# Optimization experiments

Measured on AMD Instinct MI355X. Metric: run time of the kernel, lower is better.

Reference implementation:

```python
import jax, jax.numpy as jnp
import numpy as np

B, N, DIM = 8, 2048, 1024
EPSILON = 0.03
SCALE = 1.0 / np.sqrt(DIM).astype(np.float32)


def setup_inputs() -> dict:
    key = jax.random.key(0)
    ks = jax.random.split(key, 5)
    Q = jax.random.normal(ks[0], (B, N, DIM), dtype=jnp.float32)
    K = jax.random.normal(ks[1], (B, N, DIM), dtype=jnp.float32)
    V = jax.random.normal(ks[2], (B, N, DIM), dtype=jnp.float32)
    # H_net: Linear(dim, dim//2) -> SiLU -> Linear(dim//2, 1); init like torch default scale-ish
    W1 = jax.random.normal(ks[3], (DIM, DIM // 2), dtype=jnp.float32) * (1.0 / np.sqrt(DIM))
    b1 = jnp.zeros((DIM // 2,), dtype=jnp.float32)
    W2 = jax.random.normal(ks[4], (DIM // 2, 1), dtype=jnp.float32) * (1.0 / np.sqrt(DIM // 2))
    b2 = jnp.zeros((1,), dtype=jnp.float32)
    return {"Q": Q, "K": K, "V": V, "W1": W1, "b1": b1, "W2": W2, "b2": b2}


def _mlp(x, W1, b1, W2, b2):
    h = jax.nn.silu(x @ W1 + b1)  # [B,N,dim//2]
    return h @ W2 + b2            # [B,N,1]


def reference(Q, K, V, W1, b1, W2, b2):
    def energy(q, v):
        # scores [B,N,N]
        A = jax.nn.softmax(jnp.einsum('bnd,bmd->bnm', q, K) * SCALE, axis=-1)
        attn_out = jnp.einsum('bnm,bmd->bnd', A, v)
        H = jnp.sum(_mlp(attn_out, W1, b1, W2, b2))
        return H, attn_out

    # grads of scalar energy H w.r.t. Q and V (dH_dV is computed per the
    # original code but discarded by the final split; only dH_dQ survives)
    (dH_dQ, dH_dV), attn_out = jax.grad(energy, argnums=(0, 1), has_aux=True)(Q, V)
    # S_new = cat([Q,V]) + eps*cat([dH_dV, -dH_dQ]); split -> V_new = V - eps*dH_dQ
    V_new = V - EPSILON * dH_dQ
    return V_new + attn_out
```

## Files before the change

### kernel.cpp

```cpp
#include <hip/hip_runtime.h>

typedef __bf16 bf16;
typedef __attribute__((ext_vector_type(8))) __bf16 bf16x8;
typedef __attribute__((ext_vector_type(4))) float f32x4;

#define MEMFENCE asm volatile("" ::: "memory")

__device__ __forceinline__ void gload16(const bf16* g, bf16* l) {
    __builtin_amdgcn_global_load_lds(
        (const __attribute__((address_space(1))) void*)g,
        (__attribute__((address_space(3))) void*)l,
        16, 0, 0);
}

template<int EPI>
__global__ __launch_bounds__(512, 1)
void gemm8p(const bf16* __restrict__ A, const bf16* __restrict__ Bm,
            void* __restrict__ Cp, int Kdim, int lda, int ldb, int ldc,
            long sA, long sB, long sC, float alpha,
            const float* __restrict__ aux1, const bf16* __restrict__ aux3)
{
    __shared__ __align__(16) char smem[163840];

    const int gx = gridDim.x, gy = gridDim.y;
    int lin = blockIdx.x + gx * (blockIdx.y + gy * blockIdx.z);
    const int q = (gx * gy * gridDim.z) >> 3;
    lin = (lin & 7) * q + (lin >> 3);
    const int bx = lin % gx;
    const int rem0 = lin / gx;
    const int by = rem0 % gy;
    const int bz = rem0 / gy;

    const int t0 = threadIdx.x;
    const int w = t0 >> 6, lane = t0 & 63;
    const int wm = w >> 2, wn = w & 3;
    const int m0 = by * 256, n0 = bx * 256;
    const long zb = bz;

    const bf16* Ab = A  + zb * sA + (size_t)m0 * lda;
    const bf16* Bb = Bm + zb * sB + (size_t)n0 * ldb;

    const int sr16 = lane >> 2;
    const int sce  = ((((lane & 3) << 4) ^ (((lane >> 5) & 1) << 5))) >> 1;
    const int r0s = (w >> 1) * 16 + sr16;
    const int c0s = (w & 1) * 32 + sce;
    const bf16* gA0 = Ab + (size_t)r0s * lda + c0s;
    const bf16* gA1 = Ab + (size_t)(128 + r0s) * lda + c0s;
    const bf16* gB0 = Bb + (size_t)r0s * ldb + c0s;
    const bf16* gB1 = Bb + (size_t)(128 + r0s) * ldb + c0s;
    const size_t a64 = (size_t)64 * lda, b64 = (size_t)64 * ldb;
    const int ldsW0 = w * 1024, ldsW1 = (8 + w) * 1024;

    const int lr = lane & 15, lkq = lane >> 4;
    const int phx = ((lane >> 3) & 1) << 5;
    const int frag_base = (lr * 64 + lkq * 16) ^ phx;
    const char* aR = smem + wm * 16384 + frag_base;
    const char* bR = smem + 98304 + (wn >> 1) * 16384 + (wn & 1) * 8192 + frag_base;

    f32x4 acc[8][4] = {};
    const int NTt = Kdim >> 6;

    auto stgA = [&](int h, int u, int off) {
        char* L = smem + off + h * 16384;
        const bf16* g = h ? gA1 : gA0;
        gload16(g + (size_t)u * 64,        (bf16*)(L + ldsW0));
        gload16(g + a64 + (size_t)u * 64,  (bf16*)(L + ldsW1));
    };
    auto stgB = [&](int h, int u, int p) {
        char* L = smem + 98304 + p * 32768 + h * 16384;
        const bf16* g = h ? gB1 : gB0;
        gload16(g + (size_t)u * 64,        (bf16*)(L + ldsW0));
        gload16(g + b64 + (size_t)u * 64,  (bf16*)(L + ldsW1));
    };

    stgA(0, 0, 0);     stgA(1, 0, 0);     stgB(0, 0, 0); stgB(1, 0, 0);
    stgA(0, 1, 32768); stgA(1, 1, 32768); stgB(0, 1, 1); stgB(1, 1, 1);
    asm volatile("s_waitcnt vmcnt(8)" ::: "memory");
    __builtin_amdgcn_s_barrier();
    MEMFENCE;

    bf16x8 a[4][2], bl[2][2], bh[2][2];
    #pragma unroll
    for (int mf = 0; mf < 4; ++mf)
        #pragma unroll
        for (int ks = 0; ks < 2; ++ks)
            a[mf][ks] = *(const bf16x8*)(aR + (mf * 2 + ks) * 1024);
    #pragma unroll
    for (int nf = 0; nf < 2; ++nf)
        #pragma unroll
        for (int ks = 0; ks < 2; ++ks)
            bh[nf][ks] = *(const bf16x8*)(bR + ((2 + nf) * 2 + ks) * 1024);

#define QUADQ(MFB, NFB, AARR, BARR)                                                     \
    __builtin_amdgcn_s_setprio(1);                                                      \
    _Pragma("unroll")                                                                   \
    for (int ks = 0; ks < 2; ++ks)                                                      \
        _Pragma("unroll")                                                               \
        for (int mf = 0; mf < 4; ++mf)                                                  \
            _Pragma("unroll")                                                           \
            for (int nf = 0; nf < 2; ++nf)                                              \
                acc[(MFB) + mf][(NFB) + nf] = __builtin_amdgcn_mfma_f32_16x16x32_bf16(  \
                    AARR[mf][ks], BARR[nf][ks], acc[(MFB) + mf][(NFB) + nf], 0, 0, 0);  \
    __builtin_amdgcn_s_setprio(0);

    int aOff = 0, aOff1 = 32768, sOff = 65536;
    for (int u = 0; u < NTt; ++u) {
        const int p = u & 1;
        const char* aP  = aR + aOff;
        const char* aP1 = aR + aOff1;
        const char* bP  = bR + p * 32768;
        const char* bP1 = bR + (p ^ 1) * 32768;
        const bool st2 = (u + 2 < NTt), nx = (u + 1 < NTt);

        if (st2) stgA(0, u + 2, sOff);
        #pragma unroll
        for (int nf = 0; nf < 2; ++nf)
            #pragma unroll
            for (int ks = 0; ks < 2; ++ks)
                bl[nf][ks] = *(const bf16x8*)(bP + (nf * 2 + ks) * 1024);
        QUADQ(0, 2, a, bh)

        if (st2) stgA(1, u + 2, sOff);
        QUADQ(0, 0, a, bl)
        #pragma unroll
        for (int mf = 0; mf < 4; ++mf)
            #pragma unroll
            for (int ks = 0; ks < 2; ++ks)
                a[mf][ks] = *(const bf16x8*)(aP + ((4 + mf) * 2 + ks) * 1024);
        MEMFENCE;
        if (st2)     asm volatile("s_waitcnt vmcnt(4)" ::: "memory");
        else if (nx) asm volatile("s_waitcnt vmcnt(0)" ::: "memory");
        __builtin_amdgcn_s_barrier();
        MEMFENCE;

        if (st2) stgB(0, u + 2, p);
        QUADQ(4, 0, a, bl)

        if (st2) stgB(1, u + 2, p);
        QUADQ(4, 2, a, bh)
        if (nx) {
            #pragma unroll
            for (int mf = 0; mf < 4; ++mf)
                #pragma unroll
                for (int ks = 0; ks < 2; ++ks)
                    a[mf][ks] = *(const bf16x8*)(aP1 + (mf * 2 + ks) * 1024);
            #pragma unroll
            for (int nf = 0; nf < 2; ++nf)
                #pragma unroll
                for (int ks = 0; ks < 2; ++ks)
                    bh[nf][ks] = *(const bf16x8*)(bP1 + ((2 + nf) * 2 + ks) * 1024);
        }
        MEMFENCE;
        __builtin_amdgcn_s_barrier();
        MEMFENCE;

        const int tmp = aOff; aOff = aOff1; aOff1 = sOff; sOff = tmp;
    }
#undef QUADQ

    const int rb  = m0 + wm * 128 + lkq * 4;
    const int cb0 = n0 + wn * 64 + lr;
    #pragma unroll
    for (int mf = 0; mf < 8; ++mf) {
        #pragma unroll
        for (int r = 0; r < 4; ++r) {
            const int rw = rb + mf * 16 + r;
            float rd = 0.f;
            if (EPI == 1) rd = aux1[zb * 2048 + rw];
            #pragma unroll
            for (int nf = 0; nf < 4; ++nf) {
                const int c = cb0 + nf * 16;
                const size_t ix = (size_t)rw * ldc + c;
                const float v = acc[mf][nf][r];
                if (EPI == 0) {
                    ((bf16*)Cp + zb * sC)[ix] = (bf16)(alpha * v);
                } else if (EPI == 1) {
                    bf16* Cb = (bf16*)Cp + zb * sC;
                    const bf16* Am = aux3 + zb * sC;
                    Cb[ix] = (bf16)((float)Am[ix] * (v - rd));
                } else {
                    float* C = (float*)Cp + zb * sC;
                    const float* Vv = aux1 + zb * sC;
                    const bf16* AOv = aux3 + zb * sC;
                    C[ix] = Vv[ix] + (float)AOv[ix] - alpha * v;
                }
            }
        }
    }
}

template<int EPI, int NF>
__global__ __launch_bounds__(512, 1)
void gemm_nc(const bf16* __restrict__ A, const bf16* __restrict__ Bm,
             void* __restrict__ Cp, int Kdim, int lda, int ldb, int ldc,
             long sA, long sB, long sC, float alpha,
             const float* __restrict__ aux1, const float* __restrict__ aux2,
             const bf16* __restrict__ aux3)
{
    constexpr int SB = NF * 4096;
    __shared__ __align__(16) char smem[65536 + 4 * SB];

    const int gx = gridDim.x, gy = gridDim.y;
    int lin = blockIdx.x + gx * (blockIdx.y + gy * blockIdx.z);
    const int q = (gx * gy * gridDim.z) >> 3;
    lin = (lin & 7) * q + (lin >> 3);
    const int bx = lin % gx;
    const int rem0 = lin / gx;
    const int by = rem0 % gy;
    const int bz = rem0 / gy;

    const int t0 = threadIdx.x;
    const int w = t0 >> 6, lane = t0 & 63;
    const int wm = w >> 2, wn = w & 3;
    const int m0 = by * 256, n0 = bx * (64 * NF);
    const long zb = bz;

    const bf16* Ab = A  + zb * sA + (size_t)m0 * lda;
    const bf16* Bb = Bm + zb * sB + (size_t)n0 * ldb;

    const int sr16 = lane >> 2;
    const int sce  = ((((lane & 3) << 4) ^ (((lane >> 5) & 1) << 5))) >> 1;
    const int stg0 = w * 2, stg1 = w * 2 + 1;
    const bf16* pA0 = Ab + (size_t)(stg0 * 16 + sr16) * lda + sce;
    const bf16* pA1 = Ab + (size_t)(stg1 * 16 + sr16) * lda + sce;
    const bf16* pB0 = Bb + (size_t)((NF == 4 ? stg0 : w) * 16 + sr16) * ldb + sce;
    const bf16* pB1 = Bb + (size_t)(stg1 * 16 + sr16) * ldb + sce;

    const int lr = lane & 15, lkq = lane >> 4;
    const int phx = ((lane >> 3) & 1) << 5;
    const int frag_base = lr * 64 + lkq * 16;

    f32x4 acc[8][NF] = {};
    const int NT = Kdim >> 5;

    auto issueSlot = [&](int p) {
        char* lA = smem + (p & 3) * 16384;
        char* lB = smem + 65536 + (p & 3) * SB;
        const int kt = p << 5;
        gload16(pA0 + kt, (bf16*)(lA + stg0 * 1024));
        gload16(pA1 + kt, (bf16*)(lA + stg1 * 1024));
        if (NF == 4) {
            gload16(pB0 + kt, (bf16*)(lB + stg0 * 1024));
            gload16(pB1 + kt, (bf16*)(lB + stg1 * 1024));
        } else {
            gload16(pB0 + kt, (bf16*)(lB + w * 1024));
        }
    };
    auto rdA = [&](const char* base, int sub) {
        return *(const bf16x8*)(base + (((sub << 10) + frag_base) ^ phx));
    };

    issueSlot(0); issueSlot(1); issueSlot(2);
    if (NF == 4) asm volatile("s_waitcnt vmcnt(4)" ::: "memory");
    else         asm volatile("s_waitcnt vmcnt(3)" ::: "memory");
    __builtin_amdgcn_s_barrier();
    MEMFENCE;

    bf16x8 alo[4], ahi[4], b0[NF], b1[NF];
    {
        const char* cA = smem;
        const char* cB = smem + 65536;
        #pragma unroll
        for (int mf = 0; mf < 4; ++mf) alo[mf] = rdA(cA, wm * 8 + mf);
        #pragma unroll
        for (int nf = 0; nf < NF; ++nf) b0[nf] = rdA(cB, wn * NF + nf);
    }

    auto stepBody = [&](int SL, int s, bf16x8 (&bA)[NF], bf16x8 (&bB)[NF]) {
        if (s + 3 < NT) issueSlot(s + 3);
        const char* cA = smem + SL * 16384;
        #pragma unroll
        for (int mf = 0; mf < 4; ++mf) ahi[mf] = rdA(cA, wm * 8 + 4 + mf);

        __builtin_amdgcn_s_setprio(1);
        #pragma unroll
        for (int mf = 0; mf < 4; ++mf)
            #pragma unroll
            for (int nf = 0; nf < NF; ++nf)
                acc[mf][nf] = __builtin_amdgcn_mfma_f32_16x16x32_bf16(alo[mf], bA[nf], acc[mf][nf], 0, 0, 0);
        __builtin_amdgcn_s_setprio(0);

        if (s + 1 < NT) {
            const int NS = (SL + 1) & 3;
            const char* nA = smem + NS * 16384;
            const char* nB = smem + 65536 + NS * SB;
            #pragma unroll
            for (int mf = 0; mf < 4; ++mf) alo[mf] = rdA(nA, wm * 8 + mf);
            #pragma unroll
            for (int nf = 0; nf < NF; ++nf) bB[nf] = rdA(nB, wn * NF + nf);
        }

        __builtin_amdgcn_s_setprio(1);
        #pragma unroll
        for (int mf = 0; mf < 4; ++mf)
            #pragma unroll
            for (int nf = 0; nf < NF; ++nf)
                acc[4 + mf][nf] = __builtin_amdgcn_mfma_f32_16x16x32_bf16(ahi[mf], bA[nf], acc[4 + mf][nf], 0, 0, 0);
        __builtin_amdgcn_s_setprio(0);

        MEMFENCE;
        if (s + 3 < NT) {
            if (NF == 4) asm volatile("s_waitcnt vmcnt(4)" ::: "memory");
            else         asm volatile("s_waitcnt vmcnt(3)" ::: "memory");
        } else {
            asm volatile("s_waitcnt vmcnt(0)" ::: "memory");
        }
        __builtin_amdgcn_s_barrier();
        MEMFENCE;
    };

    for (int s = 0; s < NT; s += 2) {
        stepBody(s & 3, s, b0, b1);
        stepBody((s + 1) & 3, s + 1, b1, b0);
    }

    const int rb  = m0 + wm * 128 + lkq * 4;
    const int cb0 = n0 + wn * (NF * 16) + lr;
    #pragma unroll
    for (int mf = 0; mf < 8; ++mf) {
        #pragma unroll
        for (int nf = 0; nf < NF; ++nf) {
            const int c = cb0 + nf * 16;
            #pragma unroll
            for (int r = 0; r < 4; ++r) {
                const int rw = rb + mf * 16 + r;
                const size_t ix = (size_t)rw * ldc + c;
                const float v = acc[mf][nf][r];
                if (EPI == 0) {
                    ((bf16*)Cp + zb * sC)[ix] = (bf16)(alpha * v);
                } else {
                    const float u = v + aux1[c];
                    const float sg = 1.f / (1.f + __expf(-u));
                    const float dd = sg * (1.f + u * (1.f - sg));
                    ((bf16*)Cp)[ix] = (bf16)(dd * aux2[c]);
                    ((bf16*)aux3)[ix] = (bf16)v;
                }
            }
        }
    }
}

template<bool DN, bool DT>
__global__ __launch_bounds__(256)
void transcast_k(const float* __restrict__ in, bf16* __restrict__ outN,
                 bf16* __restrict__ outT, int R, int C)
{
    __shared__ float ts[64][65];
    const int t = threadIdx.x;
    const int c0 = blockIdx.x * 64, r0 = blockIdx.y * 64;
    const size_t zoff = (size_t)blockIdx.z * R * C;

    const int rr = t >> 2, cc = (t & 3) * 16;
    float4 f[4];
    const float* src = in + zoff + (size_t)(r0 + rr) * C + c0 + cc;
    #pragma unroll
    for (int i = 0; i < 4; ++i) f[i] = *(const float4*)(src + 4 * i);

    if (DN) {
        bf16x8 h0, h1;
        #pragma unroll
        for (int i = 0; i < 2; ++i) {
            h0[i*4+0] = (bf16)f[i].x;   h0[i*4+1] = (bf16)f[i].y;
            h0[i*4+2] = (bf16)f[i].z;   h0[i*4+3] = (bf16)f[i].w;
            h1[i*4+0] = (bf16)f[i+2].x; h1[i*4+1] = (bf16)f[i+2].y;
            h1[i*4+2] = (bf16)f[i+2].z; h1[i*4+3] = (bf16)f[i+2].w;
        }
        bf16* dst = outN + zoff + (size_t)(r0 + rr) * C + c0 + cc;
        *(bf16x8*)dst = h0;
        *(bf16x8*)(dst + 8) = h1;
    }
    if (DT) {
        #pragma unroll
        for (int i = 0; i < 4; ++i) {
            ts[rr][cc + 4*i + 0] = f[i].x;
            ts[rr][cc + 4*i + 1] = f[i].y;
            ts[rr][cc + 4*i + 2] = f[i].z;
            ts[rr][cc + 4*i + 3] = f[i].w;
        }
        __syncthreads();
        const int ct = t >> 2, rr4 = (t & 3) * 16;
        bf16x8 o0, o1;
        #pragma unroll
        for (int i = 0; i < 8; ++i) o0[i] = (bf16)ts[rr4 + i][ct];
        #pragma unroll
        for (int i = 0; i < 8; ++i) o1[i] = (bf16)ts[rr4 + 8 + i][ct];
        bf16* dst = outT + zoff + (size_t)(c0 + ct) * R + r0 + rr4;
        *(bf16x8*)dst = o0;
        *(bf16x8*)(dst + 8) = o1;
    }
}

__global__ __launch_bounds__(256)
void softmax_k(const bf16* __restrict__ S, bf16* __restrict__ A)
{
    const size_t row = blockIdx.x;
    const int t = threadIdx.x;
    const int wid = t >> 6, lane = t & 63;
    __shared__ float r1[4], r2[4];

    bf16x8 v = *(const bf16x8*)(S + row * 2048 + t * 8);
    float f[8];
    float mx = -1e30f;
    #pragma unroll
    for (int i = 0; i < 8; ++i) { f[i] = (float)v[i]; mx = fmaxf(mx, f[i]); }
    #pragma unroll
    for (int o = 32; o; o >>= 1) mx = fmaxf(mx, __shfl_xor(mx, o, 64));
    if (!lane) r1[wid] = mx;
    __syncthreads();
    mx = fmaxf(fmaxf(r1[0], r1[1]), fmaxf(r1[2], r1[3]));

    float sum = 0.f;
    #pragma unroll
    for (int i = 0; i < 8; ++i) { f[i] = __expf(f[i] - mx); sum += f[i]; }
    #pragma unroll
    for (int o = 32; o; o >>= 1) sum += __shfl_xor(sum, o, 64);
    if (!lane) r2[wid] = sum;
    __syncthreads();
    sum = r2[0] + r2[1] + r2[2] + r2[3];

    const float inv = 1.f / sum;
    bf16x8 ov;
    #pragma unroll
    for (int i = 0; i < 8; ++i) ov[i] = (bf16)(f[i] * inv);
    *(bf16x8*)(A + row * 2048 + t * 8) = ov;
}

__global__ __launch_bounds__(256)
void rowdot_k(const bf16* __restrict__ U, const bf16* __restrict__ H, float* __restrict__ rd)
{
    const int r = blockIdx.x * 4 + (threadIdx.x >> 6);
    const int lane = threadIdx.x & 63;
    bf16x8 uv = *(const bf16x8*)(U + (size_t)r * 512 + lane * 8);
    bf16x8 hv = *(const bf16x8*)(H + (size_t)r * 512 + lane * 8);
    float d = 0.f;
    #pragma unroll
    for (int i = 0; i < 8; ++i) d += (float)uv[i] * (float)hv[i];
    #pragma unroll
    for (int o = 32; o; o >>= 1) d += __shfl_xor(d, o, 64);
    if (!lane) rd[r] = d;
}

extern "C" void kernel_launch(void* const* d_in, const int* in_sizes, int n_in,
                              void* d_out, int out_size, void* d_ws, size_t ws_size,
                              hipStream_t stream)
{
    const float* Q  = (const float*)d_in[0];
    const float* Km = (const float*)d_in[1];
    const float* V  = (const float*)d_in[2];
    const float* W1 = (const float*)d_in[3];
    const float* b1 = (const float*)d_in[4];
    const float* W2 = (const float*)d_in[5];
    float* out = (float*)d_out;

    char* ws = (char*)d_ws;
    bf16* Amat = (bf16*)(ws);
    bf16* AO   = (bf16*)(ws + 67108864);
    bf16* Kb   = AO;
    bf16* KbT  = (bf16*)(ws + 100663296);
    bf16* Vb   = (bf16*)(ws + 134217728);
    bf16* Hb   = Vb;
    bf16* VbT  = (bf16*)(ws + 167772160);
    bf16* U    = VbT;
    bf16* Qb   = (bf16*)(ws + 201326592);
    bf16* VW1b = Qb;
    bf16* W1T  = (bf16*)(ws + 234881024);
    float* rowdot = (float*)(ws + 235929600);
    bf16* S    = (bf16*)d_out;

    const long sQK = 2048L * 1024;
    const long sS  = 2048L * 2048;
    const long sVW = 2048L * 512;
    dim3 blk(256), blkG(512);

    transcast_k<true,  false><<<dim3(16, 32, 8), blk, 0, stream>>>(Q,  Qb, nullptr, 2048, 1024);
    transcast_k<true,  true ><<<dim3(16, 32, 8), blk, 0, stream>>>(Km, Kb, KbT,     2048, 1024);
    transcast_k<true,  true ><<<dim3(16, 32, 8), blk, 0, stream>>>(V,  Vb, VbT,     2048, 1024);
    transcast_k<false, true ><<<dim3(8,  16, 1), blk, 0, stream>>>(W1, nullptr, W1T, 1024, 512);

    gemm8p<0><<<dim3(8, 8, 8), blkG, 0, stream>>>(
        Qb, Kb, S, 1024, 1024, 1024, 2048, sQK, sQK, sS, 0.03125f, nullptr, nullptr);

    gemm_nc<0, 2><<<dim3(4, 8, 8), blkG, 0, stream>>>(
        Vb, W1T, VW1b, 1024, 1024, 1024, 512, sQK, 0, sVW, 1.0f, nullptr, nullptr, nullptr);

    softmax_k<<<dim3(16384), blk, 0, stream>>>(S, Amat);

    gemm8p<0><<<dim3(4, 8, 8), blkG, 0, stream>>>(
        Amat, VbT, AO, 2048, 2048, 2048, 1024, sS, sQK, sQK, 1.0f, nullptr, nullptr);

    gemm_nc<3, 2><<<dim3(4, 64, 1), blkG, 0, stream>>>(
        AO, W1T, U, 1024, 1024, 1024, 512, 0, 0, 0, 1.0f, b1, W2, Hb);

    rowdot_k<<<dim3(4096), blk, 0, stream>>>(U, Hb, rowdot);

    gemm8p<1><<<dim3(8, 8, 8), blkG, 0, stream>>>(
        U, VW1b, Amat, 512, 512, 512, 2048, sVW, sVW, sS, 1.0f, rowdot, Amat);

    gemm8p<2><<<dim3(4, 8, 8), blkG, 0, stream>>>(
        Amat, KbT, out, 2048, 2048, 2048, 1024, sS, sQK, sQK, 0.03f * 0.03125f, V, AO);
}
```

Baseline: 420.3 us.

## Fuse rowdot into MLP gemm epilogue and merge transcast launches

The MLP-gradient gemm epilogue now computes per-row partial dot products of U with the pre-activation directly from registers. It reduces them across lanes and waves through shared memory and writes per-column-block partials to a slab, which the next gemm's epilogue sums. This removes the separate rowdot kernel and the bf16 write and reload of H. The four transpose/cast launches are also merged into one grid, cutting launch overhead. The trade-off is an extra epilogue reduction with a barrier, and the dot product now uses fp32 pre-activation values instead of bf16-rounded ones.

```diff
diff --git a/kernel.cpp b/kernel.cpp
--- a/kernel.cpp
+++ b/kernel.cpp
@@ -166,7 +166,10 @@
         for (int r = 0; r < 4; ++r) {
             const int rw = rb + mf * 16 + r;
             float rd = 0.f;
-            if (EPI == 1) rd = aux1[zb * 2048 + rw];
+            if (EPI == 1) {
+                const size_t gr = zb * 2048 + rw;
+                rd = aux1[gr] + aux1[16384 + gr] + aux1[32768 + gr] + aux1[49152 + gr];
+            }
             #pragma unroll
             for (int nf = 0; nf < 4; ++nf) {
                 const int c = cb0 + nf * 16;
@@ -195,7 +198,7 @@
              void* __restrict__ Cp, int Kdim, int lda, int ldb, int ldc,
              long sA, long sB, long sC, float alpha,
              const float* __restrict__ aux1, const float* __restrict__ aux2,
-             const bf16* __restrict__ aux3)
+             float* __restrict__ rds)
 {
     constexpr int SB = NF * 4096;
     __shared__ __align__(16) char smem[65536 + 4 * SB];
@@ -316,39 +319,61 @@
 
     const int rb  = m0 + wm * 128 + lkq * 4;
     const int cb0 = n0 + wn * (NF * 16) + lr;
-    #pragma unroll
-    for (int mf = 0; mf < 8; ++mf) {
-        #pragma unroll
-        for (int nf = 0; nf < NF; ++nf) {
-            const int c = cb0 + nf * 16;
+
+    if (EPI == 0) {
+        #pragma unroll
+        for (int mf = 0; mf < 8; ++mf)
+            #pragma unroll
+            for (int nf = 0; nf < NF; ++nf) {
+                const int c = cb0 + nf * 16;
+                #pragma unroll
+                for (int r = 0; r < 4; ++r) {
+                    const int rw = rb + mf * 16 + r;
+                    ((bf16*)Cp + zb * sC)[(size_t)rw * ldc + c] = (bf16)(alpha * acc[mf][nf][r]);
+                }
+            }
+    } else {
+        float* smemF = (float*)smem;
+        #pragma unroll
+        for (int mf = 0; mf < 8; ++mf) {
             #pragma unroll
             for (int r = 0; r < 4; ++r) {
                 const int rw = rb + mf * 16 + r;
-                const size_t ix = (size_t)rw * ldc + c;
-                const float v = acc[mf][nf][r];
-                if (EPI == 0) {
-                    ((bf16*)Cp + zb * sC)[ix] = (bf16)(alpha * v);
-                } else {
+                float pd = 0.f;
+                #pragma unroll
+                for (int nf = 0; nf < NF; ++nf) {
+                    const int c = cb0 + nf * 16;
+                    const float v = acc[mf][nf][r];
                     const float u = v + aux1[c];
                     const float sg = 1.f / (1.f + __expf(-u));
                     const float dd = sg * (1.f + u * (1.f - sg));
-                    ((bf16*)Cp)[ix] = (bf16)(dd * aux2[c]);
-                    ((bf16*)aux3)[ix] = (bf16)v;
+                    const float uval = dd * aux2[c];
+                    ((bf16*)Cp)[(size_t)rw * ldc + c] = (bf16)uval;
+                    pd += uval * v;
                 }
+                #pragma unroll
+                for (int o = 1; o < 16; o <<= 1) pd += __shfl_xor(pd, o, 64);
+                if (lr == 0)
+                    smemF[wn * 256 + wm * 128 + mf * 16 + lkq * 4 + r] = pd;
             }
         }
+        __syncthreads();
+        if (t0 < 256) {
+            const float s4 = smemF[t0] + smemF[256 + t0] + smemF[512 + t0] + smemF[768 + t0];
+            rds[(size_t)bx * 16384 + m0 + t0] = s4;
+        }
     }
 }
 
 template<bool DN, bool DT>
-__global__ __launch_bounds__(256)
-void transcast_k(const float* __restrict__ in, bf16* __restrict__ outN,
-                 bf16* __restrict__ outT, int R, int C)
+__device__ __forceinline__ void transcast_body(
+                 const float* __restrict__ in, bf16* __restrict__ outN,
+                 bf16* __restrict__ outT, int R, int C, int bx, int by, int bz,
+                 float (*ts)[65])
 {
-    __shared__ float ts[64][65];
     const int t = threadIdx.x;
-    const int c0 = blockIdx.x * 64, r0 = blockIdx.y * 64;
-    const size_t zoff = (size_t)blockIdx.z * R * C;
+    const int c0 = bx * 64, r0 = by * 64;
+    const size_t zoff = (size_t)bz * R * C;
 
     const int rr = t >> 2, cc = (t & 3) * 16;
     float4 f[4];
@@ -387,6 +412,26 @@
         bf16* dst = outT + zoff + (size_t)(c0 + ct) * R + r0 + rr4;
         *(bf16x8*)dst = o0;
         *(bf16x8*)(dst + 8) = o1;
+    }
+}
+
+__global__ __launch_bounds__(256)
+void trans_all(const float* __restrict__ Q, const float* __restrict__ Km,
+               const float* __restrict__ V, const float* __restrict__ W1,
+               bf16* __restrict__ Qb, bf16* __restrict__ Kb, bf16* __restrict__ KbT,
+               bf16* __restrict__ Vb, bf16* __restrict__ VbT, bf16* __restrict__ W1T)
+{
+    __shared__ float ts[64][65];
+    const int z = blockIdx.z;
+    if (z < 8) {
+        transcast_body<true, false>(Q, Qb, nullptr, 2048, 1024, blockIdx.x, blockIdx.y, z, ts);
+    } else if (z < 16) {
+        transcast_body<true, true>(Km, Kb, KbT, 2048, 1024, blockIdx.x, blockIdx.y, z - 8, ts);
+    } else if (z < 24) {
+        transcast_body<true, true>(V, Vb, VbT, 2048, 1024, blockIdx.x, blockIdx.y, z - 16, ts);
+    } else {
+        if (blockIdx.x < 8 && blockIdx.y < 16)
+            transcast_body<false, true>(W1, nullptr, W1T, 1024, 512, blockIdx.x, blockIdx.y, 0, ts);
     }
 }
 
@@ -423,21 +468,6 @@
     #pragma unroll
     for (int i = 0; i < 8; ++i) ov[i] = (bf16)(f[i] * inv);
     *(bf16x8*)(A + row * 2048 + t * 8) = ov;
-}
-
-__global__ __launch_bounds__(256)
-void rowdot_k(const bf16* __restrict__ U, const bf16* __restrict__ H, float* __restrict__ rd)
-{
-    const int r = blockIdx.x * 4 + (threadIdx.x >> 6);
-    const int lane = threadIdx.x & 63;
-    bf16x8 uv = *(const bf16x8*)(U + (size_t)r * 512 + lane * 8);
-    bf16x8 hv = *(const bf16x8*)(H + (size_t)r * 512 + lane * 8);
-    float d = 0.f;
-    #pragma unroll
-    for (int i = 0; i < 8; ++i) d += (float)uv[i] * (float)hv[i];
-    #pragma unroll
-    for (int o = 32; o; o >>= 1) d += __shfl_xor(d, o, 64);
-    if (!lane) rd[r] = d;
 }
 
 extern "C" void kernel_launch(void* const* d_in, const int* in_sizes, int n_in,
@@ -458,13 +488,12 @@
     bf16* Kb   = AO;
     bf16* KbT  = (bf16*)(ws + 100663296);
     bf16* Vb   = (bf16*)(ws + 134217728);
-    bf16* Hb   = Vb;
+    float* rdSlab = (float*)(ws + 134217728);
     bf16* VbT  = (bf16*)(ws + 167772160);
     bf16* U    = VbT;
     bf16* Qb   = (bf16*)(ws + 201326592);
     bf16* VW1b = Qb;
     bf16* W1T  = (bf16*)(ws + 234881024);
-    float* rowdot = (float*)(ws + 235929600);
     bf16* S    = (bf16*)d_out;
 
     const long sQK = 2048L * 1024;
@@ -472,10 +501,7 @@
     const long sVW = 2048L * 512;
     dim3 blk(256), blkG(512);
 
-    transcast_k<true,  false><<<dim3(16, 32, 8), blk, 0, stream>>>(Q,  Qb, nullptr, 2048, 1024);
-    transcast_k<true,  true ><<<dim3(16, 32, 8), blk, 0, stream>>>(Km, Kb, KbT,     2048, 1024);
-    transcast_k<true,  true ><<<dim3(16, 32, 8), blk, 0, stream>>>(V,  Vb, VbT,     2048, 1024);
-    transcast_k<false, true ><<<dim3(8,  16, 1), blk, 0, stream>>>(W1, nullptr, W1T, 1024, 512);
+    trans_all<<<dim3(16, 32, 25), blk, 0, stream>>>(Q, Km, V, W1, Qb, Kb, KbT, Vb, VbT, W1T);
 
     gemm8p<0><<<dim3(8, 8, 8), blkG, 0, stream>>>(
         Qb, Kb, S, 1024, 1024, 1024, 2048, sQK, sQK, sS, 0.03125f, nullptr, nullptr);
@@ -489,12 +515,10 @@
         Amat, VbT, AO, 2048, 2048, 2048, 1024, sS, sQK, sQK, 1.0f, nullptr, nullptr);
 
     gemm_nc<3, 2><<<dim3(4, 64, 1), blkG, 0, stream>>>(
-        AO, W1T, U, 1024, 1024, 1024, 512, 0, 0, 0, 1.0f, b1, W2, Hb);
-
-    rowdot_k<<<dim3(4096), blk, 0, stream>>>(U, Hb, rowdot);
+        AO, W1T, U, 1024, 1024, 1024, 512, 0, 0, 0, 1.0f, b1, W2, rdSlab);
 
     gemm8p<1><<<dim3(8, 8, 8), blkG, 0, stream>>>(
-        U, VW1b, Amat, 512, 512, 512, 2048, sVW, sVW, sS, 1.0f, rowdot, Amat);
+        U, VW1b, Amat, 512, 512, 512, 2048, sVW, sVW, sS, 1.0f, rdSlab, Amat);
 
     gemm8p<2><<<dim3(4, 8, 8), blkG, 0, stream>>>(
         Amat, KbT, out, 2048, 2048, 2048, 1024, sS, sQK, sQK, 0.03f * 0.03125f, V, AO);
```

Result: faster. 405.6 us (-3.5%).
